# Kernel tuning notes

Measured on AMD Instinct MI355X. Metric: run time of the kernel, lower is better.

Reference implementation:

```python
import jax, jax.numpy as jnp
import numpy as np

N_NODES = 50000
N_EDGES = 600000
IN_DIM = 128
HID = 128
HEADS = 2
OUT_DIM = 1
NEG_SLOPE = 0.2  # PyG GATv2Conv default leaky_relu slope


def _gatv2_layer(x, src, dst, Wl, bl, Wr, br, att, bias):
    """GATv2Conv (PyG semantics): lin_l on source, lin_r on target,
    e = att . leaky_relu(xs_j + xd_i), softmax over incoming edges of i,
    out_i = sum_j alpha_ij * xs_j, heads concatenated, plus output bias."""
    n = x.shape[0]
    xs = (x @ Wl + bl).reshape(n, HEADS, HID)   # [N,H,C] source transform
    xd = (x @ Wr + br).reshape(n, HEADS, HID)   # [N,H,C] target transform
    m = xs[src] + xd[dst]                        # [E,H,C] per-edge message
    m = jnp.where(m > 0, m, NEG_SLOPE * m)       # leaky_relu
    e = jnp.einsum('ehc,hc->eh', m, att)         # [E,H] attention logits
    emax = jax.lax.stop_gradient(
        jax.ops.segment_max(e, dst, num_segments=n))  # stable softmax shift
    a = jnp.exp(e - emax[dst])
    denom = jax.ops.segment_sum(a, dst, num_segments=n)  # [N,H]
    alpha = a / (denom[dst] + 1e-16)             # [E,H] per-dest softmax
    out = jax.ops.segment_sum(alpha[:, :, None] * xs[src], dst, num_segments=n)
    return out.reshape(n, HEADS * HID) + bias


def setup_inputs() -> dict:
    key = jax.random.key(0)
    ks = jax.random.split(key, 16)
    x = jax.random.normal(ks[0], (N_NODES, IN_DIM), dtype=jnp.float32)
    edge_index = jax.random.randint(ks[1], (2, N_EDGES), 0, N_NODES, dtype=jnp.int64)

    def lin(k, fi, fo):
        s = 1.0 / np.sqrt(fi)
        k1, k2 = jax.random.split(k)
        return (jax.random.uniform(k1, (fi, fo), jnp.float32, -s, s),
                jax.random.uniform(k2, (fo,), jnp.float32, -s, s))

    Wl1, bl1 = lin(ks[2], IN_DIM, HEADS * HID)
    Wr1, br1 = lin(ks[3], IN_DIM, HEADS * HID)
    att1 = jax.random.normal(ks[4], (HEADS, HID), jnp.float32) * (1.0 / np.sqrt(HID))
    bias1 = jnp.zeros((HEADS * HID,), jnp.float32)
    Wl2, bl2 = lin(ks[5], HEADS * HID, HEADS * HID)
    Wr2, br2 = lin(ks[6], HEADS * HID, HEADS * HID)
    att2 = jax.random.normal(ks[7], (HEADS, HID), jnp.float32) * (1.0 / np.sqrt(HID))
    bias2 = jnp.zeros((HEADS * HID,), jnp.float32)
    W3, b3 = lin(ks[8], HEADS * HID, HID)
    W4, b4 = lin(ks[9], HID, OUT_DIM)
    return {"x": x, "edge_index": edge_index,
            "Wl1": Wl1, "bl1": bl1, "Wr1": Wr1, "br1": br1, "att1": att1, "bias1": bias1,
            "Wl2": Wl2, "bl2": bl2, "Wr2": Wr2, "br2": br2, "att2": att2, "bias2": bias2,
            "W3": W3, "b3": b3, "W4": W4, "b4": b4}


def reference(x, edge_index, Wl1, bl1, Wr1, br1, att1, bias1,
              Wl2, bl2, Wr2, br2, att2, bias2, W3, b3, W4, b4):
    n = x.shape[0]
    loops = jnp.arange(n, dtype=edge_index.dtype)  # add_self_loops=True (PyG default)
    src = jnp.concatenate([edge_index[0], loops])
    dst = jnp.concatenate([edge_index[1], loops])
    h = _gatv2_layer(x, src, dst, Wl1, bl1, Wr1, br1, att1, bias1)
    h = jax.nn.relu(h)  # dropout = identity in eval mode
    h = _gatv2_layer(h, src, dst, Wl2, bl2, Wr2, br2, att2, bias2)
    h = jax.nn.relu(h)
    h = (h @ W3 + b3) @ W4 + b4  # post_mp: Linear -> Dropout(id) -> Linear
    return jax.nn.sigmoid(h)
```

## Files before the change

### kernel.cpp

```cpp
#include <hip/hip_runtime.h>
#include <hip/hip_bf16.h>
#include <math.h>


typedef short bf16x8 __attribute__((ext_vector_type(8)));
typedef float f32x4  __attribute__((ext_vector_type(4)));

#define TM 128
#define TN 128
#define GBK 64

__device__ inline void load_lds16(const void* g, void* l)
{
    __builtin_amdgcn_global_load_lds((const __attribute__((address_space(1))) void*)g,
                                     (__attribute__((address_space(3))) void*)l, 16, 0, 0);
}

__global__ __launch_bounds__(256) void gemm_mfma(
    const __hip_bfloat16* __restrict__ A, const __hip_bfloat16* __restrict__ Bt,
    const float* __restrict__ bl, const float* __restrict__ br,
    float* __restrict__ C, int M, int K, int ldc)
{
    __shared__ char lsA[TM * GBK * 2];
    __shared__ char lsB[TN * GBK * 2];

    int t = threadIdx.x;
    int w = t >> 6, l = t & 63;
    int row0 = blockIdx.y * TM;
    int col0 = blockIdx.x * TN;

    int wrow = (w >> 1) * 64, wcol = (w & 1) * 64;
    int lr = l & 15, lh = l >> 4;

    f32x4 acc[4][4] = {};

    for (int k0 = 0; k0 < K; k0 += GBK) {
#pragma unroll
        for (int c = 0; c < 4; ++c) {
            int i = c * 256 + t;
            int r = i >> 3, p = i & 7;
            int sl = p ^ (r & 7);
            load_lds16(A  + (size_t)(row0 + r) * K + k0 + sl * 8, lsA + (c * 256 + w * 64) * 16);
            load_lds16(Bt + (size_t)(col0 + r) * K + k0 + sl * 8, lsB + (c * 256 + w * 64) * 16);
        }
        __syncthreads();
#pragma unroll
        for (int kk = 0; kk < 2; ++kk) {
            bf16x8 af[4], bg[4];
#pragma unroll
            for (int m = 0; m < 4; ++m) {
                int r = wrow + m * 16 + lr;
                int sl = (kk * 4 + lh) ^ (r & 7);
                af[m] = *(const bf16x8*)(lsA + r * 128 + sl * 16);
            }
#pragma unroll
            for (int n = 0; n < 4; ++n) {
                int r = wcol + n * 16 + lr;
                int sl = (kk * 4 + lh) ^ (r & 7);
                bg[n] = *(const bf16x8*)(lsB + r * 128 + sl * 16);
            }
#pragma unroll
            for (int m = 0; m < 4; ++m)
#pragma unroll
                for (int n = 0; n < 4; ++n)
                    acc[m][n] = __builtin_amdgcn_mfma_f32_16x16x32_bf16(af[m], bg[n], acc[m][n], 0, 0, 0);
        }
        __syncthreads();
    }

#pragma unroll
    for (int n = 0; n < 4; ++n) {
        int col = col0 + wcol + n * 16 + lr;
        float bv = (col < 256) ? bl[col] : br[col - 256];
#pragma unroll
        for (int m = 0; m < 4; ++m) {
            int rbase = row0 + wrow + m * 16 + lh * 4;
#pragma unroll
            for (int j = 0; j < 4; ++j) {
                int row = rbase + j;
                if (row < M) C[(size_t)row * ldc + col] = acc[m][n][j] + bv;
            }
        }
    }
}


__global__ void prep_wt(const float* __restrict__ Wl, const float* __restrict__ Wr,
                        __hip_bfloat16* __restrict__ Wt, int K)
{
    int idx = blockIdx.x * blockDim.x + threadIdx.x;
    if (idx >= 512 * K) return;
    int n = idx / K, k = idx - n * K;
    float v = (n < 256) ? Wl[(size_t)k * 256 + n] : Wr[(size_t)k * 256 + (n - 256)];
    Wt[idx] = __float2bfloat16(v);
}

__global__ void conv_bf16(const float* __restrict__ in, __hip_bfloat16* __restrict__ out, int n)
{
    int i = blockIdx.x * blockDim.x + threadIdx.x;
    if (i * 4 >= n) return;
    float4 v = *(const float4*)&in[i * 4];
    __hip_bfloat16 t0 = __float2bfloat16(v.x), t1 = __float2bfloat16(v.y);
    __hip_bfloat16 t2 = __float2bfloat16(v.z), t3 = __float2bfloat16(v.w);
    ushort4 pk = make_ushort4(*(unsigned short*)&t0, *(unsigned short*)&t1,
                              *(unsigned short*)&t2, *(unsigned short*)&t3);
    *(ushort4*)&out[(size_t)i * 4] = pk;
}


__global__ void count_edges(const int* __restrict__ dst, int* __restrict__ counts, int E)
{
    int i = blockIdx.x * blockDim.x + threadIdx.x;
    if (i < E) atomicAdd(&counts[dst[i]], 1);
}

__global__ __launch_bounds__(1024) void scan_kernel(
    const int* __restrict__ counts, int* __restrict__ row_ptr,
    int* __restrict__ cursor, int n)
{
    __shared__ int wsum[16];
    __shared__ int stot;
    int tid = threadIdx.x;
    int lane = tid & 63, wid = tid >> 6;
    int offset = 0;
    for (int base = 0; base < n; base += 1024) {
        int idx = base + tid;
        int v = (idx < n) ? counts[idx] : 0;
        int x = v;
#pragma unroll
        for (int off = 1; off < 64; off <<= 1) {
            int y = __shfl_up(x, off);
            if (lane >= off) x += y;
        }
        if (lane == 63) wsum[wid] = x;
        __syncthreads();
        if (tid == 0) {
            int run = 0;
#pragma unroll
            for (int i = 0; i < 16; ++i) { int tt = wsum[i]; wsum[i] = run; run += tt; }
            stot = run;
        }
        __syncthreads();
        int excl = offset + wsum[wid] + x - v;
        if (idx < n) { row_ptr[idx] = excl; cursor[idx] = excl; }
        offset += stot;
        __syncthreads();
    }
    if (tid == 0) row_ptr[n] = offset;
}

__global__ void scatter_edges(const int* __restrict__ src, const int* __restrict__ dst,
                              int* __restrict__ cursor, int* __restrict__ csr_src, int E)
{
    int i = blockIdx.x * blockDim.x + threadIdx.x;
    if (i < E) {
        int pos = atomicAdd(&cursor[dst[i]], 1);
        csr_src[pos] = src[i];
    }
}

__global__ __launch_bounds__(256) void w34_kernel(
    const float* __restrict__ W3, const float* __restrict__ b3,
    const float* __restrict__ W4, const float* __restrict__ b4,
    float* __restrict__ w34)
{
    int wid = blockIdx.x * 4 + (threadIdx.x >> 6);
    int lane = threadIdx.x & 63;
    if (wid > 256) return;
    const float* row = (wid < 256) ? &W3[(size_t)wid * 128] : b3;
    float p = row[lane] * W4[lane] + row[lane + 64] * W4[lane + 64];
#pragma unroll
    for (int off = 32; off; off >>= 1) p += __shfl_xor(p, off);
    if (lane == 0) w34[wid] = (wid < 256) ? p : (p + b4[0]);
}


template<bool FUSED>
__global__ __launch_bounds__(256) void gat_agg(
    const float* __restrict__ xsd,
    const float* __restrict__ att, const float* __restrict__ bias,
    const int* __restrict__ row_ptr, const int* __restrict__ csr_src,
    __hip_bfloat16* __restrict__ outb, float* __restrict__ outf,
    const float* __restrict__ w34, int n)
{
    int node = blockIdx.x * 4 + (threadIdx.x >> 6);
    if (node >= n) return;
    int lane = threadIdx.x & 63;
    int c = lane * 4;

    float4 xdv = *(const float4*)&xsd[(size_t)node * 512 + 256 + c];
    float4 atv = *(const float4*)&att[c];

    float m = -INFINITY, l = 0.f;
    float4 acc = make_float4(0.f, 0.f, 0.f, 0.f);

    int s = row_ptr[node], e = row_ptr[node + 1];
    int deg = e - s;
    int my_src = (lane < deg) ? csr_src[s + lane] : 0;

    for (int i = -1; i < deg; ++i) {
        int srcn = (i < 0) ? node : ((i < 64) ? __shfl(my_src, i) : csr_src[s + i]);
        float4 xv = *(const float4*)&xsd[(size_t)srcn * 512 + c];
        float v0 = xv.x + xdv.x; v0 = v0 > 0.f ? v0 : 0.2f * v0;
        float v1 = xv.y + xdv.y; v1 = v1 > 0.f ? v1 : 0.2f * v1;
        float v2 = xv.z + xdv.z; v2 = v2 > 0.f ? v2 : 0.2f * v2;
        float v3 = xv.w + xdv.w; v3 = v3 > 0.f ? v3 : 0.2f * v3;
        float p = v0 * atv.x + v1 * atv.y + v2 * atv.z + v3 * atv.w;
#pragma unroll
        for (int off = 16; off; off >>= 1) p += __shfl_xor(p, off);
        float mn = fmaxf(m, p);
        float sc = __expf(m - mn);
        float wgt = __expf(p - mn);
        l = l * sc + wgt;
        acc.x = acc.x * sc + wgt * xv.x;
        acc.y = acc.y * sc + wgt * xv.y;
        acc.z = acc.z * sc + wgt * xv.z;
        acc.w = acc.w * sc + wgt * xv.w;
        m = mn;
    }
    float inv = 1.f / (l + 1e-16f);
    float4 bv = *(const float4*)&bias[c];
    float4 o;
    o.x = fmaxf(acc.x * inv + bv.x, 0.f);
    o.y = fmaxf(acc.y * inv + bv.y, 0.f);
    o.z = fmaxf(acc.z * inv + bv.z, 0.f);
    o.w = fmaxf(acc.w * inv + bv.w, 0.f);

    if (!FUSED) {
        __hip_bfloat16 t0 = __float2bfloat16(o.x), t1 = __float2bfloat16(o.y);
        __hip_bfloat16 t2 = __float2bfloat16(o.z), t3 = __float2bfloat16(o.w);
        ushort4 pk = make_ushort4(*(unsigned short*)&t0, *(unsigned short*)&t1,
                                  *(unsigned short*)&t2, *(unsigned short*)&t3);
        *(ushort4*)&outb[(size_t)node * 256 + c] = pk;
    } else {
        float4 wv = *(const float4*)&w34[c];
        float p = o.x * wv.x + o.y * wv.y + o.z * wv.z + o.w * wv.w;
#pragma unroll
        for (int off = 32; off; off >>= 1) p += __shfl_xor(p, off);
        if (lane == 0) outf[node] = 1.f / (1.f + __expf(-(p + w34[256])));
    }
}


extern "C" void kernel_launch(void* const* d_in, const int* in_sizes, int n_in,
                              void* d_out, int out_size, void* d_ws, size_t ws_size,
                              hipStream_t stream)
{
    const float* x     = (const float*)d_in[0];
    const int*   ei    = (const int*)d_in[1];
    const float* Wl1   = (const float*)d_in[2];
    const float* bl1   = (const float*)d_in[3];
    const float* Wr1   = (const float*)d_in[4];
    const float* br1   = (const float*)d_in[5];
    const float* att1  = (const float*)d_in[6];
    const float* bias1 = (const float*)d_in[7];
    const float* Wl2   = (const float*)d_in[8];
    const float* bl2   = (const float*)d_in[9];
    const float* Wr2   = (const float*)d_in[10];
    const float* br2   = (const float*)d_in[11];
    const float* att2  = (const float*)d_in[12];
    const float* bias2 = (const float*)d_in[13];
    const float* W3    = (const float*)d_in[14];
    const float* b3    = (const float*)d_in[15];
    const float* W4    = (const float*)d_in[16];
    const float* b4    = (const float*)d_in[17];

    const int N = in_sizes[0] / 128;
    const int E = in_sizes[1] / 2;
    const int Mp = ((N + TM - 1) / TM) * TM;
    const int* src = ei;
    const int* dst = ei + E;

    char* ws = (char*)d_ws;
    float*          xsd     = (float*)(ws + 0);
    __hip_bfloat16* xbf     = (__hip_bfloat16*)(ws + 102400000);
    __hip_bfloat16* hbf     = (__hip_bfloat16*)(ws + 115212544);
    __hip_bfloat16* Wt1     = (__hip_bfloat16*)(ws + 140837120);
    __hip_bfloat16* Wt2     = (__hip_bfloat16*)(ws + 140968192);
    int*            row_ptr = (int*)(ws + 141230336);
    int*            counts  = (int*)(ws + 141430400);
    int*            cursor  = (int*)(ws + 141630400);
    int*            csr_src = (int*)(ws + 141830400);
    float*          w34     = (float*)(ws + 144230400);

    hipMemsetAsync(counts, 0, N * sizeof(int), stream);
    count_edges<<<(E + 255) / 256, 256, 0, stream>>>(dst, counts, E);
    scan_kernel<<<1, 1024, 0, stream>>>(counts, row_ptr, cursor, N);
    scatter_edges<<<(E + 255) / 256, 256, 0, stream>>>(src, dst, cursor, csr_src, E);
    w34_kernel<<<65, 256, 0, stream>>>(W3, b3, W4, b4, w34);
    prep_wt<<<(512 * 128 + 255) / 256, 256, 0, stream>>>(Wl1, Wr1, Wt1, 128);
    prep_wt<<<(512 * 256 + 255) / 256, 256, 0, stream>>>(Wl2, Wr2, Wt2, 256);
    conv_bf16<<<(N * 128 / 4 + 255) / 256, 256, 0, stream>>>(x, xbf, N * 128);

    dim3 gemmGrid(512 / TN, Mp / TM);
    int aggBlocks = (N + 3) / 4;

    gemm_mfma<<<gemmGrid, 256, 0, stream>>>(xbf, Wt1, bl1, br1, xsd, N, 128, 512);
    gat_agg<false><<<aggBlocks, 256, 0, stream>>>(xsd, att1, bias1, row_ptr, csr_src,
                                                  hbf, nullptr, nullptr, N);

    gemm_mfma<<<gemmGrid, 256, 0, stream>>>(hbf, Wt2, bl2, br2, xsd, N, 256, 512);
    gat_agg<true><<<aggBlocks, 256, 0, stream>>>(xsd, att2, bias2, row_ptr, csr_src,
                                                 nullptr, (float*)d_out, w34, N);
}
```

Measured before the change: 497.5 us.

## Store source features as fp16 and use lazy max rescaling in online softmax

The GEMM epilogue now writes the source-side transform as fp16 into its own array and the target-side transform as fp32 into a separate array. This halves the bytes of the per-edge gather in the aggregation kernels. The online softmax also skips the rescale exponentials whenever every lane's new logit is within 8 of the running max. This cuts exp work per edge, at the cost of fp16 rounding on gathered features and slightly larger unnormalised accumulators.

```diff
diff --git a/kernel.cpp b/kernel.cpp
--- a/kernel.cpp
+++ b/kernel.cpp
@@ -1,5 +1,6 @@
 #include <hip/hip_runtime.h>
 #include <hip/hip_bf16.h>
+#include <hip/hip_fp16.h>
 #include <math.h>
 
 
@@ -19,7 +20,8 @@
 __global__ __launch_bounds__(256) void gemm_mfma(
     const __hip_bfloat16* __restrict__ A, const __hip_bfloat16* __restrict__ Bt,
     const float* __restrict__ bl, const float* __restrict__ br,
-    float* __restrict__ C, int M, int K, int ldc)
+    _Float16* __restrict__ xsh, float* __restrict__ xd,
+    int M, int K)
 {
     __shared__ char lsA[TM * GBK * 2];
     __shared__ char lsB[TN * GBK * 2];
@@ -68,17 +70,22 @@
         __syncthreads();
     }
 
+    bool is_xs = (col0 < 256);
 #pragma unroll
     for (int n = 0; n < 4; ++n) {
         int col = col0 + wcol + n * 16 + lr;
-        float bv = (col < 256) ? bl[col] : br[col - 256];
+        float bv = is_xs ? bl[col] : br[col - 256];
 #pragma unroll
         for (int m = 0; m < 4; ++m) {
             int rbase = row0 + wrow + m * 16 + lh * 4;
 #pragma unroll
             for (int j = 0; j < 4; ++j) {
                 int row = rbase + j;
-                if (row < M) C[(size_t)row * ldc + col] = acc[m][n][j] + bv;
+                if (row < M) {
+                    float v = acc[m][n][j] + bv;
+                    if (is_xs) xsh[(size_t)row * 256 + col] = (_Float16)v;
+                    else       xd [(size_t)row * 256 + col - 256] = v;
+                }
             }
         }
     }
@@ -177,7 +184,7 @@
 
 template<bool FUSED>
 __global__ __launch_bounds__(256) void gat_agg(
-    const float* __restrict__ xsd,
+    const _Float16* __restrict__ xsh, const float* __restrict__ xd,
     const float* __restrict__ att, const float* __restrict__ bias,
     const int* __restrict__ row_ptr, const int* __restrict__ csr_src,
     __hip_bfloat16* __restrict__ outb, float* __restrict__ outf,
@@ -188,7 +195,7 @@
     int lane = threadIdx.x & 63;
     int c = lane * 4;
 
-    float4 xdv = *(const float4*)&xsd[(size_t)node * 512 + 256 + c];
+    float4 xdv = *(const float4*)&xd[(size_t)node * 256 + c];
     float4 atv = *(const float4*)&att[c];
 
     float m = -INFINITY, l = 0.f;
@@ -200,23 +207,38 @@
 
     for (int i = -1; i < deg; ++i) {
         int srcn = (i < 0) ? node : ((i < 64) ? __shfl(my_src, i) : csr_src[s + i]);
-        float4 xv = *(const float4*)&xsd[(size_t)srcn * 512 + c];
-        float v0 = xv.x + xdv.x; v0 = v0 > 0.f ? v0 : 0.2f * v0;
-        float v1 = xv.y + xdv.y; v1 = v1 > 0.f ? v1 : 0.2f * v1;
-        float v2 = xv.z + xdv.z; v2 = v2 > 0.f ? v2 : 0.2f * v2;
-        float v3 = xv.w + xdv.w; v3 = v3 > 0.f ? v3 : 0.2f * v3;
+        ushort4 us = *(const ushort4*)&xsh[(size_t)srcn * 256 + c];
+        float x0 = (float)(*(const _Float16*)&us.x);
+        float x1 = (float)(*(const _Float16*)&us.y);
+        float x2 = (float)(*(const _Float16*)&us.z);
+        float x3 = (float)(*(const _Float16*)&us.w);
+        float v0 = x0 + xdv.x; v0 = v0 > 0.f ? v0 : 0.2f * v0;
+        float v1 = x1 + xdv.y; v1 = v1 > 0.f ? v1 : 0.2f * v1;
+        float v2 = x2 + xdv.z; v2 = v2 > 0.f ? v2 : 0.2f * v2;
+        float v3 = x3 + xdv.w; v3 = v3 > 0.f ? v3 : 0.2f * v3;
         float p = v0 * atv.x + v1 * atv.y + v2 * atv.z + v3 * atv.w;
 #pragma unroll
         for (int off = 16; off; off >>= 1) p += __shfl_xor(p, off);
-        float mn = fmaxf(m, p);
-        float sc = __expf(m - mn);
-        float wgt = __expf(p - mn);
-        l = l * sc + wgt;
-        acc.x = acc.x * sc + wgt * xv.x;
-        acc.y = acc.y * sc + wgt * xv.y;
-        acc.z = acc.z * sc + wgt * xv.z;
-        acc.w = acc.w * sc + wgt * xv.w;
-        m = mn;
+
+        float pm = p - m;
+        if (__all(pm <= 8.f)) {
+            float wgt = __expf(pm);
+            l += wgt;
+            acc.x += wgt * x0;
+            acc.y += wgt * x1;
+            acc.z += wgt * x2;
+            acc.w += wgt * x3;
+        } else {
+            float mn = fmaxf(m, p);
+            float sc = __expf(m - mn);
+            float wgt = __expf(p - mn);
+            l = l * sc + wgt;
+            acc.x = acc.x * sc + wgt * x0;
+            acc.y = acc.y * sc + wgt * x1;
+            acc.z = acc.z * sc + wgt * x2;
+            acc.w = acc.w * sc + wgt * x3;
+            m = mn;
+        }
     }
     float inv = 1.f / (l + 1e-16f);
     float4 bv = *(const float4*)&bias[c];
@@ -272,16 +294,17 @@
     const int* dst = ei + E;
 
     char* ws = (char*)d_ws;
-    float*          xsd     = (float*)(ws + 0);
-    __hip_bfloat16* xbf     = (__hip_bfloat16*)(ws + 102400000);
-    __hip_bfloat16* hbf     = (__hip_bfloat16*)(ws + 115212544);
-    __hip_bfloat16* Wt1     = (__hip_bfloat16*)(ws + 140837120);
-    __hip_bfloat16* Wt2     = (__hip_bfloat16*)(ws + 140968192);
-    int*            row_ptr = (int*)(ws + 141230336);
-    int*            counts  = (int*)(ws + 141430400);
-    int*            cursor  = (int*)(ws + 141630400);
-    int*            csr_src = (int*)(ws + 141830400);
-    float*          w34     = (float*)(ws + 144230400);
+    _Float16*       xsh     = (_Float16*)(ws + 0);
+    float*          xd      = (float*)(ws + 25600000);
+    __hip_bfloat16* xbf     = (__hip_bfloat16*)(ws + 76800000);
+    __hip_bfloat16* hbf     = (__hip_bfloat16*)(ws + 89612288);
+    __hip_bfloat16* Wt1     = (__hip_bfloat16*)(ws + 115236864);
+    __hip_bfloat16* Wt2     = (__hip_bfloat16*)(ws + 115367936);
+    int*            row_ptr = (int*)(ws + 115630080);
+    int*            counts  = (int*)(ws + 115830144);
+    int*            cursor  = (int*)(ws + 116030144);
+    int*            csr_src = (int*)(ws + 116230144);
+    float*          w34     = (float*)(ws + 118630144);
 
     hipMemsetAsync(counts, 0, N * sizeof(int), stream);
     count_edges<<<(E + 255) / 256, 256, 0, stream>>>(dst, counts, E);
@@ -295,11 +318,11 @@
     dim3 gemmGrid(512 / TN, Mp / TM);
     int aggBlocks = (N + 3) / 4;
 
-    gemm_mfma<<<gemmGrid, 256, 0, stream>>>(xbf, Wt1, bl1, br1, xsd, N, 128, 512);
-    gat_agg<false><<<aggBlocks, 256, 0, stream>>>(xsd, att1, bias1, row_ptr, csr_src,
+    gemm_mfma<<<gemmGrid, 256, 0, stream>>>(xbf, Wt1, bl1, br1, xsh, xd, N, 128);
+    gat_agg<false><<<aggBlocks, 256, 0, stream>>>(xsh, xd, att1, bias1, row_ptr, csr_src,
                                                   hbf, nullptr, nullptr, N);
 
-    gemm_mfma<<<gemmGrid, 256, 0, stream>>>(hbf, Wt2, bl2, br2, xsd, N, 256, 512);
-    gat_agg<true><<<aggBlocks, 256, 0, stream>>>(xsd, att2, bias2, row_ptr, csr_src,
+    gemm_mfma<<<gemmGrid, 256, 0, stream>>>(hbf, Wt2, bl2, br2, xsh, xd, N, 256);
+    gat_agg<true><<<aggBlocks, 256, 0, stream>>>(xsh, xd, att2, bias2, row_ptr, csr_src,
                                                  nullptr, (float*)d_out, w34, N);
 }
```

Measured after the change: 476.5 us. 1.04x faster.
